# Kernel optimization log

Hardware: AMD Instinct MI355X
Metric: run time of the kernel (lower is better)

## Reference

```python
import jax, jax.numpy as jnp
from jax import lax
import numpy as np


def _depthwise_conv(x, k2d):
    # x: [B, C, H, W]; k2d: [kh, kw] applied identically to every channel (SAME padding)
    C = x.shape[1]
    kern = jnp.broadcast_to(k2d[None, None], (C, 1) + k2d.shape)  # [C,1,kh,kw]
    return lax.conv_general_dilated(
        x, kern, window_strides=(1, 1), padding='SAME',
        dimension_numbers=('NCHW', 'OIHW', 'NCHW'), feature_group_count=C)


def setup_inputs() -> dict:
    key = jax.random.key(0)
    img = jax.random.uniform(key, (32, 3, 512, 512), dtype=jnp.float32)
    # gaussian(5, std=1.0) from scipy: exp(-0.5 * ((i-2)/1)^2)
    gauss = jnp.asarray(np.exp(-0.5 * (np.arange(5) - 2.0) ** 2), dtype=jnp.float32)
    sobel = jnp.asarray([[1., 0., -1.], [2., 0., -2.], [1., 0., -1.]], dtype=jnp.float32)
    return {"img": img, "gauss": gauss, "sobel": sobel}


def reference(img, gauss, sobel):
    # separable Gaussian blur: 1x5 horizontal then 5x1 vertical, per channel
    blur = _depthwise_conv(_depthwise_conv(img, gauss[None, :]), gauss[:, None])
    # Sobel gradients per channel
    gx = _depthwise_conv(blur, sobel)      # horizontal sobel
    gy = _depthwise_conv(blur, sobel.T)    # vertical sobel
    # magnitude summed over the 3 color channels -> [B,1,H,W]
    grad_mag = jnp.sqrt(jnp.sum(gx * gx + gy * gy, axis=1, keepdims=True))
    return grad_mag / jnp.max(grad_mag)
```

## Files before the change

kernel.cpp:

```cpp
#include <hip/hip_runtime.h>
#include <math.h>

#define HH 512
#define WW 512
#define TH 16
#define NROWS 18
#define NLOAD 22
#define VBW 520

__global__ __launch_bounds__(256, 3)
void edge_fused_v2(const float* __restrict__ img,
                   const float* __restrict__ gauss,
                   float* __restrict__ out,
                   unsigned int* __restrict__ gmax) {
    __shared__ float vb[NROWS][VBW];
    __shared__ float s_red[4];

    const int tid = threadIdx.x;
    const int bid = blockIdx.x;
    const int strip = bid & 31;
    const int b     = bid >> 5;
    const int ry0 = strip * TH;
    const int c0  = tid * 2;

    const float g0 = gauss[0], g1 = gauss[1], g2 = gauss[2], g3 = gauss[3], g4 = gauss[4];

    if (tid < 72) {
        const int r = tid >> 2, k = tid & 3;
        vb[r][(k < 2) ? k : 512 + k] = 0.f;
    }

    const bool interior = (ry0 >= 3) && (ry0 + TH + 3 <= HH);

    float acc0[TH], acc1[TH];
#pragma unroll
    for (int o = 0; o < TH; ++o) { acc0[o] = 0.f; acc1[o] = 0.f; }

    for (int c = 0; c < 3; ++c) {
        const float* imgc = img + ((size_t)(b * 3 + c) * HH) * WW;

        float2 w[NLOAD];
        if (interior) {
#pragma unroll
            for (int i = 0; i < NLOAD; ++i)
                w[i] = *(const float2*)(imgc + (size_t)(ry0 - 3 + i) * WW + c0);
        } else {
#pragma unroll
            for (int i = 0; i < NLOAD; ++i) {
                const int y = ry0 - 3 + i;
                w[i] = (y >= 0 && y < HH)
                     ? *(const float2*)(imgc + (size_t)y * WW + c0)
                     : make_float2(0.f, 0.f);
            }
        }
#pragma unroll
        for (int r = 0; r < NROWS; ++r) {
            float2 s;
            s.x = g0*w[r].x + g1*w[r+1].x + g2*w[r+2].x + g3*w[r+3].x + g4*w[r+4].x;
            s.y = g0*w[r].y + g1*w[r+1].y + g2*w[r+2].y + g3*w[r+3].y + g4*w[r+4].y;
            *(float2*)&vb[r][c0 + 2] = s;
        }
        __syncthreads();

        float2 bl[NROWS];
#pragma unroll
        for (int r = 0; r < NROWS; ++r) {
            const float2 A  = *(const float2*)&vb[r][c0];
            const float2 Bv = *(const float2*)&vb[r][c0 + 2];
            const float2 C  = *(const float2*)&vb[r][c0 + 4];
            bl[r].x = g0*A.x  + g1*A.y  + g2*Bv.x + g3*Bv.y + g4*C.x;
            bl[r].y = g0*A.y  + g1*Bv.x + g2*Bv.y + g3*C.x  + g4*C.y;
        }
        __syncthreads();

        if (interior) {
#pragma unroll
            for (int r = 0; r < NROWS; ++r)
                *(float2*)&vb[r][c0 + 2] = bl[r];
        } else {
#pragma unroll
            for (int r = 0; r < NROWS; ++r) {
                const int yb = ry0 - 1 + r;
                float2 v = bl[r];
                if (yb < 0 || yb >= HH) { v.x = 0.f; v.y = 0.f; }
                *(float2*)&vb[r][c0 + 2] = v;
            }
        }
        __syncthreads();

        float u0[2], v0[2], u1[2], v1[2];
#pragma unroll
        for (int r = 0; r < 2; ++r) {
            const float2 A  = *(const float2*)&vb[r][c0];
            const float2 Bv = *(const float2*)&vb[r][c0 + 2];
            const float2 C  = *(const float2*)&vb[r][c0 + 4];
            u0[r] = A.y - Bv.y;   v0[r] = A.y  + 2.f*Bv.x + Bv.y;
            u1[r] = Bv.x - C.x;   v1[r] = Bv.x + 2.f*Bv.y + C.x;
        }
#pragma unroll
        for (int o = 0; o < TH; ++o) {
            const int r = o + 2;
            const float2 A  = *(const float2*)&vb[r][c0];
            const float2 Bv = *(const float2*)&vb[r][c0 + 2];
            const float2 C  = *(const float2*)&vb[r][c0 + 4];
            const float nu0 = A.y - Bv.y,  nv0 = A.y  + 2.f*Bv.x + Bv.y;
            const float nu1 = Bv.x - C.x,  nv1 = Bv.x + 2.f*Bv.y + C.x;
            const float gx0 = u0[0] + 2.f*u0[1] + nu0;
            const float gy0 = v0[0] - nv0;
            const float gx1 = u1[0] + 2.f*u1[1] + nu1;
            const float gy1 = v1[0] - nv1;
            acc0[o] += gx0*gx0 + gy0*gy0;
            acc1[o] += gx1*gx1 + gy1*gy1;
            u0[0] = u0[1]; u0[1] = nu0;  v0[0] = v0[1]; v0[1] = nv0;
            u1[0] = u1[1]; u1[1] = nu1;  v1[0] = v1[1]; v1[1] = nv1;
        }
        __syncthreads();
    }

    float m = 0.f;
#pragma unroll
    for (int o = 0; o < TH; ++o) {
        float2 v;
        v.x = sqrtf(acc0[o]);
        v.y = sqrtf(acc1[o]);
        *(float2*)(out + ((size_t)b * HH + (ry0 + o)) * WW + c0) = v;
        m = fmaxf(m, fmaxf(v.x, v.y));
    }
#pragma unroll
    for (int off = 32; off > 0; off >>= 1)
        m = fmaxf(m, __shfl_xor(m, off, 64));
    if ((tid & 63) == 0) s_red[tid >> 6] = m;
    __syncthreads();
    if (tid == 0) {
        const float bm = fmaxf(fmaxf(s_red[0], s_red[1]), fmaxf(s_red[2], s_red[3]));
        atomicMax(gmax, __float_as_uint(bm));
    }
}

__global__ __launch_bounds__(256)
void normalize_v2(float* __restrict__ out,
                  const unsigned int* __restrict__ gmax,
                  int n4) {
    const float inv = 1.0f / __uint_as_float(*gmax);
    float4* o4 = (float4*)out;
    const int stride = gridDim.x * blockDim.x;
    for (int i = blockIdx.x * blockDim.x + threadIdx.x; i < n4; i += stride) {
        float4 v = o4[i];
        v.x *= inv; v.y *= inv; v.z *= inv; v.w *= inv;
        o4[i] = v;
    }
}

extern "C" void kernel_launch(void* const* d_in, const int* in_sizes, int n_in,
                              void* d_out, int out_size, void* d_ws, size_t ws_size,
                              hipStream_t stream) {
    const float* img   = (const float*)d_in[0];
    const float* gauss = (const float*)d_in[1];
    float* out = (float*)d_out;

    unsigned int* gmax = (unsigned int*)d_ws;
    hipMemsetAsync(gmax, 0, sizeof(unsigned int), stream);

    const int B = 32;
    const int blocks = B * (HH / TH);
    edge_fused_v2<<<blocks, 256, 0, stream>>>(img, gauss, out, gmax);

    const int n4 = out_size / 4;
    normalize_v2<<<4096, 256, 0, stream>>>(out, gmax, n4);
}
```

Before: 175.9 us.

## Halve row tile, drop smem padding, defer sqrt into normalize pass

Cuts the strip height per block from 16 to 8 rows and raises the launch bound from 3 to 8 blocks per SM. The smaller register and shared-memory footprint is meant to allow more resident waves. The shared buffer loses its zero-padded halo columns, and edge threads now predicate their neighbour loads to zero instead. The sqrt moves from the fused kernel into the normalize pass: the max is taken on squared magnitudes and each output becomes sqrt(v*inv), which is mathematically equivalent. The trade-off is more vertical halo reloads, since 14 input rows now feed 8 output rows instead of 22 feeding 16, plus twice as many atomics.

After: 261.8 us. +48.9%, slower.

```diff
diff --git a/kernel.cpp b/kernel.cpp
--- a/kernel.cpp
+++ b/kernel.cpp
@@ -3,34 +3,31 @@
 
 #define HH 512
 #define WW 512
-#define TH 16
-#define NROWS 18
-#define NLOAD 22
-#define VBW 520
+#define TH 8
+#define NROWS 10
+#define NLOAD 14
+#define VBW 512
 
-__global__ __launch_bounds__(256, 3)
-void edge_fused_v2(const float* __restrict__ img,
+__global__ __launch_bounds__(256, 8)
+void edge_fused_v3(const float* __restrict__ img,
                    const float* __restrict__ gauss,
                    float* __restrict__ out,
                    unsigned int* __restrict__ gmax) {
     __shared__ float vb[NROWS][VBW];
-    __shared__ float s_red[4];
 
     const int tid = threadIdx.x;
     const int bid = blockIdx.x;
-    const int strip = bid & 31;
-    const int b     = bid >> 5;
+    const int strip = bid & 63;
+    const int b     = bid >> 6;
     const int ry0 = strip * TH;
     const int c0  = tid * 2;
 
     const float g0 = gauss[0], g1 = gauss[1], g2 = gauss[2], g3 = gauss[3], g4 = gauss[4];
 
-    if (tid < 72) {
-        const int r = tid >> 2, k = tid & 3;
-        vb[r][(k < 2) ? k : 512 + k] = 0.f;
-    }
-
     const bool interior = (ry0 >= 3) && (ry0 + TH + 3 <= HH);
+    const bool haveA = (c0 >= 2);
+    const bool haveC = (c0 < WW - 2);
+    const float2 Z = make_float2(0.f, 0.f);
 
     float acc0[TH], acc1[TH];
 #pragma unroll
@@ -50,7 +47,7 @@
                 const int y = ry0 - 3 + i;
                 w[i] = (y >= 0 && y < HH)
                      ? *(const float2*)(imgc + (size_t)y * WW + c0)
-                     : make_float2(0.f, 0.f);
+                     : Z;
             }
         }
 #pragma unroll
@@ -58,16 +55,16 @@
             float2 s;
             s.x = g0*w[r].x + g1*w[r+1].x + g2*w[r+2].x + g3*w[r+3].x + g4*w[r+4].x;
             s.y = g0*w[r].y + g1*w[r+1].y + g2*w[r+2].y + g3*w[r+3].y + g4*w[r+4].y;
-            *(float2*)&vb[r][c0 + 2] = s;
+            *(float2*)&vb[r][c0] = s;
         }
         __syncthreads();
 
         float2 bl[NROWS];
 #pragma unroll
         for (int r = 0; r < NROWS; ++r) {
-            const float2 A  = *(const float2*)&vb[r][c0];
-            const float2 Bv = *(const float2*)&vb[r][c0 + 2];
-            const float2 C  = *(const float2*)&vb[r][c0 + 4];
+            const float2 A  = haveA ? *(const float2*)&vb[r][c0 - 2] : Z;
+            const float2 Bv = *(const float2*)&vb[r][c0];
+            const float2 C  = haveC ? *(const float2*)&vb[r][c0 + 2] : Z;
             bl[r].x = g0*A.x  + g1*A.y  + g2*Bv.x + g3*Bv.y + g4*C.x;
             bl[r].y = g0*A.y  + g1*Bv.x + g2*Bv.y + g3*C.x  + g4*C.y;
         }
@@ -76,14 +73,14 @@
         if (interior) {
 #pragma unroll
             for (int r = 0; r < NROWS; ++r)
-                *(float2*)&vb[r][c0 + 2] = bl[r];
+                *(float2*)&vb[r][c0] = bl[r];
         } else {
 #pragma unroll
             for (int r = 0; r < NROWS; ++r) {
                 const int yb = ry0 - 1 + r;
                 float2 v = bl[r];
                 if (yb < 0 || yb >= HH) { v.x = 0.f; v.y = 0.f; }
-                *(float2*)&vb[r][c0 + 2] = v;
+                *(float2*)&vb[r][c0] = v;
             }
         }
         __syncthreads();
@@ -91,18 +88,18 @@
         float u0[2], v0[2], u1[2], v1[2];
 #pragma unroll
         for (int r = 0; r < 2; ++r) {
-            const float2 A  = *(const float2*)&vb[r][c0];
-            const float2 Bv = *(const float2*)&vb[r][c0 + 2];
-            const float2 C  = *(const float2*)&vb[r][c0 + 4];
+            const float2 A  = haveA ? *(const float2*)&vb[r][c0 - 2] : Z;
+            const float2 Bv = *(const float2*)&vb[r][c0];
+            const float2 C  = haveC ? *(const float2*)&vb[r][c0 + 2] : Z;
             u0[r] = A.y - Bv.y;   v0[r] = A.y  + 2.f*Bv.x + Bv.y;
             u1[r] = Bv.x - C.x;   v1[r] = Bv.x + 2.f*Bv.y + C.x;
         }
 #pragma unroll
         for (int o = 0; o < TH; ++o) {
             const int r = o + 2;
-            const float2 A  = *(const float2*)&vb[r][c0];
-            const float2 Bv = *(const float2*)&vb[r][c0 + 2];
-            const float2 C  = *(const float2*)&vb[r][c0 + 4];
+            const float2 A  = haveA ? *(const float2*)&vb[r][c0 - 2] : Z;
+            const float2 Bv = *(const float2*)&vb[r][c0];
+            const float2 C  = haveC ? *(const float2*)&vb[r][c0 + 2] : Z;
             const float nu0 = A.y - Bv.y,  nv0 = A.y  + 2.f*Bv.x + Bv.y;
             const float nu1 = Bv.x - C.x,  nv1 = Bv.x + 2.f*Bv.y + C.x;
             const float gx0 = u0[0] + 2.f*u0[1] + nu0;
@@ -120,25 +117,23 @@
     float m = 0.f;
 #pragma unroll
     for (int o = 0; o < TH; ++o) {
-        float2 v;
-        v.x = sqrtf(acc0[o]);
-        v.y = sqrtf(acc1[o]);
+        float2 v; v.x = acc0[o]; v.y = acc1[o];
         *(float2*)(out + ((size_t)b * HH + (ry0 + o)) * WW + c0) = v;
         m = fmaxf(m, fmaxf(v.x, v.y));
     }
 #pragma unroll
     for (int off = 32; off > 0; off >>= 1)
         m = fmaxf(m, __shfl_xor(m, off, 64));
-    if ((tid & 63) == 0) s_red[tid >> 6] = m;
+    if ((tid & 63) == 0) vb[0][tid >> 6] = m;
     __syncthreads();
     if (tid == 0) {
-        const float bm = fmaxf(fmaxf(s_red[0], s_red[1]), fmaxf(s_red[2], s_red[3]));
+        const float bm = fmaxf(fmaxf(vb[0][0], vb[0][1]), fmaxf(vb[0][2], vb[0][3]));
         atomicMax(gmax, __float_as_uint(bm));
     }
 }
 
 __global__ __launch_bounds__(256)
-void normalize_v2(float* __restrict__ out,
+void normalize_v3(float* __restrict__ out,
                   const unsigned int* __restrict__ gmax,
                   int n4) {
     const float inv = 1.0f / __uint_as_float(*gmax);
@@ -146,7 +141,10 @@
     const int stride = gridDim.x * blockDim.x;
     for (int i = blockIdx.x * blockDim.x + threadIdx.x; i < n4; i += stride) {
         float4 v = o4[i];
-        v.x *= inv; v.y *= inv; v.z *= inv; v.w *= inv;
+        v.x = sqrtf(v.x * inv);
+        v.y = sqrtf(v.y * inv);
+        v.z = sqrtf(v.z * inv);
+        v.w = sqrtf(v.w * inv);
         o4[i] = v;
     }
 }
@@ -163,8 +161,8 @@
 
     const int B = 32;
     const int blocks = B * (HH / TH);
-    edge_fused_v2<<<blocks, 256, 0, stream>>>(img, gauss, out, gmax);
+    edge_fused_v3<<<blocks, 256, 0, stream>>>(img, gauss, out, gmax);
 
     const int n4 = out_size / 4;
-    normalize_v2<<<4096, 256, 0, stream>>>(out, gmax, n4);
+    normalize_v3<<<4096, 256, 0, stream>>>(out, gmax, n4);
 }
```
